# Optimization experiments

Measured on AMD Instinct MI355X. Metric: run time of the kernel, lower is better.

The kernel has to match this reference:

```python
import jax, jax.numpy as jnp
import numpy as np

N_NODES = 50000
N_EDGES = 800000
D_IN = 128
HIDDEN = [128, 128]
D_OUT = 64


def setup_inputs() -> dict:
    key = jax.random.key(0)
    ks = jax.random.split(key, 12)
    x = jax.random.normal(ks[0], (N_NODES, D_IN), dtype=jnp.float32)
    edge_index = jax.random.randint(ks[1], (2, N_EDGES), 0, N_NODES, dtype=jnp.int64)
    # SAGEConv params: lin_l acts on aggregated neighbors (has bias), lin_r on root
    def lin(k, fan_in, fan_out):
        s = 1.0 / np.sqrt(fan_in)
        return jax.random.uniform(k, (fan_in, fan_out), jnp.float32, -s, s)
    dims = [D_IN] + HIDDEN
    inp = {"x": x, "edge_index": edge_index}
    for i in range(len(HIDDEN)):
        inp[f"Wl{i}"] = lin(ks[2 + 3 * i], dims[i], dims[i + 1])
        inp[f"Wr{i}"] = lin(ks[3 + 3 * i], dims[i], dims[i + 1])
        inp[f"b{i}"] = jnp.zeros((dims[i + 1],), jnp.float32)
    inp["Wfc"] = lin(ks[10], HIDDEN[-1], D_OUT)
    inp["bfc"] = jnp.zeros((D_OUT,), jnp.float32)
    return inp


def _sage_conv(x, src, dst, n, Wl, Wr, b, deg_inv):
    # mean-aggregate source features into destination nodes
    agg = jax.ops.segment_sum(x[src], dst, num_segments=n) * deg_inv[:, None]
    return agg @ Wl + x @ Wr + b


def reference(x, edge_index, Wl0, Wr0, b0, Wl1, Wr1, b1, Wfc, bfc):
    src, dst = edge_index[0], edge_index[1]
    n = x.shape[0]
    deg = jax.ops.segment_sum(jnp.ones((src.shape[0],), x.dtype), dst, num_segments=n)
    deg_inv = 1.0 / jnp.maximum(deg, 1.0)
    h = jax.nn.relu(_sage_conv(x, src, dst, n, Wl0, Wr0, b0, deg_inv))
    # dropout p=0 / eval mode -> identity
    h = jax.nn.relu(_sage_conv(h, src, dst, n, Wl1, Wr1, b1, deg_inv))
    return h @ Wfc + bfc
```

## Files before the change

### kernel.cpp

```cpp
#include <hip/hip_runtime.h>
#include <hip/hip_bf16.h>

#define NN 50000
#define NE 800000
#define D 128
#define DOUT 64
#define PAD 64
#define BSH 8
#define NBUCK 196
#define CAP 4608
#define CHUNK 4096

typedef __attribute__((ext_vector_type(8))) short short8;
typedef __attribute__((ext_vector_type(4))) float float4v;


__device__ inline unsigned short f2bf(float f) {
    union { float f; unsigned int i; } c; c.f = f;
    unsigned int u = c.i;
    return (unsigned short)((u + 0x7fffu + ((u >> 16) & 1u)) >> 16);
}
__device__ inline float bflo(unsigned int u) {
    union { unsigned int i; float f; } c; c.i = u << 16; return c.f;
}
__device__ inline float bfhi(unsigned int u) {
    union { unsigned int i; float f; } c; c.i = u & 0xffff0000u; return c.f;
}


__global__ void cast_f32_bf16(const float* __restrict__ in, unsigned short* __restrict__ outb, int n8) {
    int i = blockIdx.x * 256 + threadIdx.x;
    if (i >= n8) return;
    const float4* p = (const float4*)in + (size_t)i * 2;
    float4 a = p[0], b = p[1];
    unsigned int w0 = f2bf(a.x) | ((unsigned int)f2bf(a.y) << 16);
    unsigned int w1 = f2bf(a.z) | ((unsigned int)f2bf(a.w) << 16);
    unsigned int w2 = f2bf(b.x) | ((unsigned int)f2bf(b.y) << 16);
    unsigned int w3 = f2bf(b.z) | ((unsigned int)f2bf(b.w) << 16);
    *(uint4*)(outb + (size_t)i * 8) = make_uint4(w0, w1, w2, w3);
}


struct PackArgs {
    const float* W[5];
    unsigned short* P[5];
};

__global__ void pack_all(PackArgs args) {
    int idx = blockIdx.x * 256 + threadIdx.x;
    if (idx >= 4 * 2048 + 1024) return;
    const float* W;
    unsigned short* P;
    int COLS, local;
    if (idx < 4 * 2048) {
        int wsel = idx >> 11;
        W = args.W[wsel]; P = args.P[wsel]; COLS = 128; local = idx & 2047;
    } else {
        W = args.W[4]; P = args.P[4]; COLS = 64; local = idx - 4 * 2048;
    }
    int CT = COLS >> 4;
    int lane = local & 63;
    int fi = local >> 6;
    int ct = fi % CT;
    int kstep = fi / CT;
    int krow = kstep * 32 + (lane >> 4) * 8;
    int col = ct * 16 + (lane & 15);
    unsigned short v[8];
#pragma unroll
    for (int j = 0; j < 8; ++j) v[j] = f2bf(W[(size_t)(krow + j) * COLS + col]);
    unsigned int w0 = v[0] | ((unsigned int)v[1] << 16);
    unsigned int w1 = v[2] | ((unsigned int)v[3] << 16);
    unsigned int w2 = v[4] | ((unsigned int)v[5] << 16);
    unsigned int w3 = v[6] | ((unsigned int)v[7] << 16);
    *(uint4*)(P + (size_t)local * 8) = make_uint4(w0, w1, w2, w3);
}


__global__ void bin_edges(const int* __restrict__ src, const int* __restrict__ dst,
                          int* __restrict__ gcur, unsigned int* __restrict__ binned, int e) {
    __shared__ int cnt[NBUCK];
    __shared__ int sh[256];
    __shared__ int baseg[NBUCK];
    __shared__ int lcur[NBUCK];
    __shared__ unsigned int buf[CHUNK];
    int tid = threadIdx.x;
    int base = blockIdx.x * CHUNK;
    for (int b = tid; b < NBUCK; b += 256) cnt[b] = 0;
    __syncthreads();
    unsigned int rec[16];
#pragma unroll
    for (int i = 0; i < 16; ++i) {
        int ei = base + i * 256 + tid;
        rec[i] = 0xffffffffu;
        if (ei < e) {
            unsigned int d = (unsigned int)dst[ei];
            unsigned int s = (unsigned int)src[ei];
            rec[i] = (d << 16) | s;
            atomicAdd(&cnt[d >> BSH], 1);
        }
    }
    __syncthreads();
    int v = (tid < NBUCK) ? cnt[tid] : 0;
    sh[tid] = v;
    __syncthreads();
    for (int off = 1; off < 256; off <<= 1) {
        int t = (tid >= off) ? sh[tid - off] : 0;
        __syncthreads();
        sh[tid] += t;
        __syncthreads();
    }
    if (tid < NBUCK) {
        baseg[tid] = atomicAdd(&gcur[tid], cnt[tid]);
        lcur[tid] = sh[tid] - cnt[tid];
    }
    __syncthreads();
    int total = sh[255];
#pragma unroll
    for (int i = 0; i < 16; ++i) {
        if (rec[i] != 0xffffffffu) {
            int b = rec[i] >> 24;
            int pos = atomicAdd(&lcur[b], 1);
            buf[pos] = rec[i];
        }
    }
    __syncthreads();
    for (int j = tid; j < total; j += 256) {
        unsigned int r = buf[j];
        int b = r >> 24;
        int gidx = baseg[b] + (j - (sh[b] - cnt[b]));
        if (gidx < CAP) binned[(size_t)b * CAP + gidx] = r;
    }
}


__global__ void scatter_bucket(const unsigned int* __restrict__ binned, const int* __restrict__ gcur,
                               unsigned short* __restrict__ eidx_pad, int* __restrict__ cursor) {
    __shared__ int cur[256];
    int b = blockIdx.x;
    int tid = threadIdx.x;
    cur[tid] = 0;
    __syncthreads();
    int count = gcur[b];
    if (count > CAP) count = CAP;
    const unsigned int* seg = binned + (size_t)b * CAP;
    for (int j = tid; j < count; j += 256) {
        unsigned int r = seg[j];
        int dl = (r >> 16) & 255;
        int slot = atomicAdd(&cur[dl], 1);
        if (slot < PAD)
            eidx_pad[((size_t)((b << BSH) + dl)) * PAD + slot] = (unsigned short)(r & 0xffffu);
    }
    __syncthreads();
    int node = (b << BSH) + tid;
    if (node < NN) cursor[node] = (cur[tid] < PAD) ? cur[tid] : PAD;
}


template <bool FUSEFC>
__global__ void fused_layer(const unsigned short* __restrict__ feat,
                            const int* __restrict__ cursor, const unsigned short* __restrict__ eidx_pad,
                            const unsigned short* __restrict__ Pl, const unsigned short* __restrict__ Pr,
                            const float* __restrict__ bias,
                            const unsigned short* __restrict__ Pfc, const float* __restrict__ bfc,
                            unsigned short* __restrict__ outb, float* __restrict__ outf, int n) {
    __shared__ __align__(16) unsigned short As[64][136];
    __shared__ __align__(16) unsigned short Xs[64][136];

    int tid = threadIdx.x;
    int row0 = blockIdx.x * 64;

    for (int v = tid; v < 1024; v += 256) {
        int r = v >> 4;
        int c8 = (v & 15) * 8;
        int gr = row0 + r;
        uint4 xv = make_uint4(0, 0, 0, 0);
        if (gr < n) xv = *(const uint4*)(feat + (size_t)gr * D + c8);
        *(uint4*)&Xs[r][c8] = xv;
    }

    {
        int g = tid >> 4;
        int l = tid & 15;
#pragma unroll
        for (int nn = 0; nn < 4; ++nn) {
            int r = g * 4 + nn;
            int node = row0 + r;
            float acc[8] = {0.f, 0.f, 0.f, 0.f, 0.f, 0.f, 0.f, 0.f};
            float di = 1.f;
            if (node < n) {
                int deg = cursor[node];
                di = 1.0f / (float)(deg > 1 ? deg : 1);
                const unsigned short* rowp = eidx_pad + (size_t)node * PAD;
                int p = 0;
                for (; p + 3 < deg; p += 4) {
                    int s0 = rowp[p], s1 = rowp[p + 1], s2 = rowp[p + 2], s3 = rowp[p + 3];
                    uint4 v0 = *(const uint4*)(feat + (size_t)s0 * D + l * 8);
                    uint4 v1 = *(const uint4*)(feat + (size_t)s1 * D + l * 8);
                    uint4 v2 = *(const uint4*)(feat + (size_t)s2 * D + l * 8);
                    uint4 v3 = *(const uint4*)(feat + (size_t)s3 * D + l * 8);
                    acc[0] += (bflo(v0.x) + bflo(v1.x)) + (bflo(v2.x) + bflo(v3.x));
                    acc[1] += (bfhi(v0.x) + bfhi(v1.x)) + (bfhi(v2.x) + bfhi(v3.x));
                    acc[2] += (bflo(v0.y) + bflo(v1.y)) + (bflo(v2.y) + bflo(v3.y));
                    acc[3] += (bfhi(v0.y) + bfhi(v1.y)) + (bfhi(v2.y) + bfhi(v3.y));
                    acc[4] += (bflo(v0.z) + bflo(v1.z)) + (bflo(v2.z) + bflo(v3.z));
                    acc[5] += (bfhi(v0.z) + bfhi(v1.z)) + (bfhi(v2.z) + bfhi(v3.z));
                    acc[6] += (bflo(v0.w) + bflo(v1.w)) + (bflo(v2.w) + bflo(v3.w));
                    acc[7] += (bfhi(v0.w) + bfhi(v1.w)) + (bfhi(v2.w) + bfhi(v3.w));
                }
                for (; p < deg; ++p) {
                    int s = rowp[p];
                    uint4 v0 = *(const uint4*)(feat + (size_t)s * D + l * 8);
                    acc[0] += bflo(v0.x); acc[1] += bfhi(v0.x);
                    acc[2] += bflo(v0.y); acc[3] += bfhi(v0.y);
                    acc[4] += bflo(v0.z); acc[5] += bfhi(v0.z);
                    acc[6] += bflo(v0.w); acc[7] += bfhi(v0.w);
                }
            }
            unsigned int w0 = f2bf(acc[0] * di) | ((unsigned int)f2bf(acc[1] * di) << 16);
            unsigned int w1 = f2bf(acc[2] * di) | ((unsigned int)f2bf(acc[3] * di) << 16);
            unsigned int w2 = f2bf(acc[4] * di) | ((unsigned int)f2bf(acc[5] * di) << 16);
            unsigned int w3 = f2bf(acc[6] * di) | ((unsigned int)f2bf(acc[7] * di) << 16);
            *(uint4*)&As[r][l * 8] = make_uint4(w0, w1, w2, w3);
        }
    }
    __syncthreads();

    int wave = tid >> 6;
    int lane = tid & 63;
    int m16 = lane & 15;
    int quad = lane >> 4;
    int rt0 = (wave & 1) * 32;
    int ctb = (wave >> 1) * 4;

    float4v acc[2][4];
#pragma unroll
    for (int t = 0; t < 2; ++t)
#pragma unroll
        for (int c = 0; c < 4; ++c) acc[t][c] = (float4v){0.f, 0.f, 0.f, 0.f};

#pragma unroll
    for (int ks = 0; ks < 4; ++ks) {
        short8 af[2];
#pragma unroll
        for (int t = 0; t < 2; ++t)
            af[t] = *(const short8*)&As[rt0 + t * 16 + m16][ks * 32 + quad * 8];
#pragma unroll
        for (int c = 0; c < 4; ++c) {
            short8 bf = *(const short8*)(Pl + ((size_t)((ks * 8 + ctb + c) * 64 + lane)) * 8);
#pragma unroll
            for (int t = 0; t < 2; ++t)
                acc[t][c] = __builtin_amdgcn_mfma_f32_16x16x32_bf16(af[t], bf, acc[t][c], 0, 0, 0);
        }
    }
#pragma unroll
    for (int ks = 0; ks < 4; ++ks) {
        short8 xf[2];
#pragma unroll
        for (int t = 0; t < 2; ++t)
            xf[t] = *(const short8*)&Xs[rt0 + t * 16 + m16][ks * 32 + quad * 8];
#pragma unroll
        for (int c = 0; c < 4; ++c) {
            short8 bf = *(const short8*)(Pr + ((size_t)((ks * 8 + ctb + c) * 64 + lane)) * 8);
#pragma unroll
            for (int t = 0; t < 2; ++t)
                acc[t][c] = __builtin_amdgcn_mfma_f32_16x16x32_bf16(xf[t], bf, acc[t][c], 0, 0, 0);
        }
    }

    if (!FUSEFC) {
#pragma unroll
        for (int t = 0; t < 2; ++t) {
#pragma unroll
            for (int c = 0; c < 4; ++c) {
                int col = (ctb + c) * 16 + m16;
                float bv = bias[col];
#pragma unroll
                for (int i = 0; i < 4; ++i) {
                    int row = row0 + rt0 + t * 16 + quad * 4 + i;
                    if (row < n)
                        outb[(size_t)row * D + col] = f2bf(fmaxf(acc[t][c][i] + bv, 0.f));
                }
            }
        }
    } else {
        __syncthreads();
#pragma unroll
        for (int t = 0; t < 2; ++t) {
#pragma unroll
            for (int c = 0; c < 4; ++c) {
                int col = (ctb + c) * 16 + m16;
                float bv = bias[col];
#pragma unroll
                for (int i = 0; i < 4; ++i) {
                    int row = rt0 + t * 16 + quad * 4 + i;
                    As[row][col] = f2bf(fmaxf(acc[t][c][i] + bv, 0.f));
                }
            }
        }
        __syncthreads();

        int ctbF = (wave >> 1) * 2;
        float4v acc2[2][2];
#pragma unroll
        for (int t = 0; t < 2; ++t)
#pragma unroll
            for (int c = 0; c < 2; ++c) acc2[t][c] = (float4v){0.f, 0.f, 0.f, 0.f};
#pragma unroll
        for (int ks = 0; ks < 4; ++ks) {
            short8 hf[2];
#pragma unroll
            for (int t = 0; t < 2; ++t)
                hf[t] = *(const short8*)&As[rt0 + t * 16 + m16][ks * 32 + quad * 8];
#pragma unroll
            for (int c = 0; c < 2; ++c) {
                short8 bf = *(const short8*)(Pfc + ((size_t)((ks * 4 + ctbF + c) * 64 + lane)) * 8);
#pragma unroll
                for (int t = 0; t < 2; ++t)
                    acc2[t][c] = __builtin_amdgcn_mfma_f32_16x16x32_bf16(hf[t], bf, acc2[t][c], 0, 0, 0);
            }
        }
#pragma unroll
        for (int t = 0; t < 2; ++t) {
#pragma unroll
            for (int c = 0; c < 2; ++c) {
                int col = (ctbF + c) * 16 + m16;
                float bv = bfc[col];
#pragma unroll
                for (int i = 0; i < 4; ++i) {
                    int row = row0 + rt0 + t * 16 + quad * 4 + i;
                    if (row < n)
                        outf[(size_t)row * DOUT + col] = acc2[t][c][i] + bv;
                }
            }
        }
    }
}


extern "C" void kernel_launch(void* const* d_in, const int* in_sizes, int n_in,
                              void* d_out, int out_size, void* d_ws, size_t ws_size,
                              hipStream_t stream) {
    const float* x   = (const float*)d_in[0];
    const int*   ei  = (const int*)d_in[1];
    const float* Wl0 = (const float*)d_in[2];
    const float* Wr0 = (const float*)d_in[3];
    const float* b0  = (const float*)d_in[4];
    const float* Wl1 = (const float*)d_in[5];
    const float* Wr1 = (const float*)d_in[6];
    const float* b1  = (const float*)d_in[7];
    const float* Wfc = (const float*)d_in[8];
    const float* bfc = (const float*)d_in[9];
    float* out = (float*)d_out;

    const int* src = ei;
    const int* dst = ei + NE;

    char* p = (char*)d_ws;
    auto carve = [&](size_t bytes) {
        char* q = p;
        p += (bytes + 255) & ~(size_t)255;
        return q;
    };
    int*            cursor   = (int*)carve(NN * sizeof(int));
    int*            gcur     = (int*)carve(NBUCK * sizeof(int));
    unsigned int*   binned   = (unsigned int*)carve((size_t)NBUCK * CAP * 4);
    unsigned short* eidx_pad = (unsigned short*)carve((size_t)NN * PAD * 2);
    unsigned short* xb   = (unsigned short*)carve((size_t)NN * D * 2);
    unsigned short* h0b  = (unsigned short*)carve((size_t)NN * D * 2);
    unsigned short* Wl0p = (unsigned short*)carve(D * D * 2);
    unsigned short* Wr0p = (unsigned short*)carve(D * D * 2);
    unsigned short* Wl1p = (unsigned short*)carve(D * D * 2);
    unsigned short* Wr1p = (unsigned short*)carve(D * D * 2);
    unsigned short* Wfcp = (unsigned short*)carve(D * DOUT * 2);

    hipMemsetAsync(gcur, 0, NBUCK * sizeof(int), stream);

    const int N8 = NN * D / 8;
    cast_f32_bf16<<<(N8 + 255) / 256, 256, 0, stream>>>(x, xb, N8);

    PackArgs pa;
    pa.W[0] = Wl0; pa.W[1] = Wr0; pa.W[2] = Wl1; pa.W[3] = Wr1; pa.W[4] = Wfc;
    pa.P[0] = Wl0p; pa.P[1] = Wr0p; pa.P[2] = Wl1p; pa.P[3] = Wr1p; pa.P[4] = Wfcp;
    pack_all<<<(4 * 2048 + 1024 + 255) / 256, 256, 0, stream>>>(pa);

    const int BINB = (NE + CHUNK - 1) / CHUNK;
    bin_edges<<<BINB, 256, 0, stream>>>(src, dst, gcur, binned, NE);
    scatter_bucket<<<NBUCK, 256, 0, stream>>>(binned, gcur, eidx_pad, cursor);

    const int GB = (NN + 63) / 64;

    fused_layer<false><<<GB, 256, 0, stream>>>(xb, cursor, eidx_pad, Wl0p, Wr0p, b0,
                                               nullptr, nullptr, h0b, nullptr, NN);
    fused_layer<true><<<GB, 256, 0, stream>>>(h0b, cursor, eidx_pad, Wl1p, Wr1p, b1,
                                              Wfcp, bfc, nullptr, out, NN);
}
```

Measured before the change: 199.1 us.

## Drop Xs LDS tile, widen neighbor gather, fold gcur reset into pack kernel

Several changes at once. The Xs shared-memory tile is removed and root features are read directly from global memory as MFMA operands, which halves LDS use so more blocks fit per CU; launch bounds of 4 blocks per CU are set to match. The gather loop now loads 8 neighbor indices with one vector load and issues 8 feature loads per iteration for more memory-level parallelism. The hipMemsetAsync of the bucket counters is replaced by an extra block in pack_all, removing one launch. The risks are higher register pressure from the wider unroll and uncoalesced global reads for the root operand.

New measurement: 199.0 us. About the same (-0.1%).

```diff
diff --git a/kernel.cpp b/kernel.cpp
--- a/kernel.cpp
+++ b/kernel.cpp
@@ -44,9 +44,14 @@
 struct PackArgs {
     const float* W[5];
     unsigned short* P[5];
+    int* gcur;
 };
 
 __global__ void pack_all(PackArgs args) {
+    if (blockIdx.x == 36) {
+        if (threadIdx.x < NBUCK) args.gcur[threadIdx.x] = 0;
+        return;
+    }
     int idx = blockIdx.x * 256 + threadIdx.x;
     if (idx >= 4 * 2048 + 1024) return;
     const float* W;
@@ -157,26 +162,17 @@
 
 
 template <bool FUSEFC>
-__global__ void fused_layer(const unsigned short* __restrict__ feat,
-                            const int* __restrict__ cursor, const unsigned short* __restrict__ eidx_pad,
-                            const unsigned short* __restrict__ Pl, const unsigned short* __restrict__ Pr,
-                            const float* __restrict__ bias,
-                            const unsigned short* __restrict__ Pfc, const float* __restrict__ bfc,
-                            unsigned short* __restrict__ outb, float* __restrict__ outf, int n) {
+__global__ __launch_bounds__(256, 4)
+void fused_layer(const unsigned short* __restrict__ feat,
+                 const int* __restrict__ cursor, const unsigned short* __restrict__ eidx_pad,
+                 const unsigned short* __restrict__ Pl, const unsigned short* __restrict__ Pr,
+                 const float* __restrict__ bias,
+                 const unsigned short* __restrict__ Pfc, const float* __restrict__ bfc,
+                 unsigned short* __restrict__ outb, float* __restrict__ outf, int n) {
     __shared__ __align__(16) unsigned short As[64][136];
-    __shared__ __align__(16) unsigned short Xs[64][136];
 
     int tid = threadIdx.x;
     int row0 = blockIdx.x * 64;
-
-    for (int v = tid; v < 1024; v += 256) {
-        int r = v >> 4;
-        int c8 = (v & 15) * 8;
-        int gr = row0 + r;
-        uint4 xv = make_uint4(0, 0, 0, 0);
-        if (gr < n) xv = *(const uint4*)(feat + (size_t)gr * D + c8);
-        *(uint4*)&Xs[r][c8] = xv;
-    }
 
     {
         int g = tid >> 4;
@@ -192,8 +188,41 @@
                 di = 1.0f / (float)(deg > 1 ? deg : 1);
                 const unsigned short* rowp = eidx_pad + (size_t)node * PAD;
                 int p = 0;
-                for (; p + 3 < deg; p += 4) {
-                    int s0 = rowp[p], s1 = rowp[p + 1], s2 = rowp[p + 2], s3 = rowp[p + 3];
+                for (; p + 7 < deg; p += 8) {
+                    uint4 iv = *(const uint4*)(rowp + p);
+                    int s0 = iv.x & 0xffff, s1 = iv.x >> 16;
+                    int s2 = iv.y & 0xffff, s3 = iv.y >> 16;
+                    int s4 = iv.z & 0xffff, s5 = iv.z >> 16;
+                    int s6 = iv.w & 0xffff, s7 = iv.w >> 16;
+                    uint4 v0 = *(const uint4*)(feat + (size_t)s0 * D + l * 8);
+                    uint4 v1 = *(const uint4*)(feat + (size_t)s1 * D + l * 8);
+                    uint4 v2 = *(const uint4*)(feat + (size_t)s2 * D + l * 8);
+                    uint4 v3 = *(const uint4*)(feat + (size_t)s3 * D + l * 8);
+                    uint4 v4 = *(const uint4*)(feat + (size_t)s4 * D + l * 8);
+                    uint4 v5 = *(const uint4*)(feat + (size_t)s5 * D + l * 8);
+                    uint4 v6 = *(const uint4*)(feat + (size_t)s6 * D + l * 8);
+                    uint4 v7 = *(const uint4*)(feat + (size_t)s7 * D + l * 8);
+                    acc[0] += ((bflo(v0.x) + bflo(v1.x)) + (bflo(v2.x) + bflo(v3.x)))
+                            + ((bflo(v4.x) + bflo(v5.x)) + (bflo(v6.x) + bflo(v7.x)));
+                    acc[1] += ((bfhi(v0.x) + bfhi(v1.x)) + (bfhi(v2.x) + bfhi(v3.x)))
+                            + ((bfhi(v4.x) + bfhi(v5.x)) + (bfhi(v6.x) + bfhi(v7.x)));
+                    acc[2] += ((bflo(v0.y) + bflo(v1.y)) + (bflo(v2.y) + bflo(v3.y)))
+                            + ((bflo(v4.y) + bflo(v5.y)) + (bflo(v6.y) + bflo(v7.y)));
+                    acc[3] += ((bfhi(v0.y) + bfhi(v1.y)) + (bfhi(v2.y) + bfhi(v3.y)))
+                            + ((bfhi(v4.y) + bfhi(v5.y)) + (bfhi(v6.y) + bfhi(v7.y)));
+                    acc[4] += ((bflo(v0.z) + bflo(v1.z)) + (bflo(v2.z) + bflo(v3.z)))
+                            + ((bflo(v4.z) + bflo(v5.z)) + (bflo(v6.z) + bflo(v7.z)));
+                    acc[5] += ((bfhi(v0.z) + bfhi(v1.z)) + (bfhi(v2.z) + bfhi(v3.z)))
+                            + ((bfhi(v4.z) + bfhi(v5.z)) + (bfhi(v6.z) + bfhi(v7.z)));
+                    acc[6] += ((bflo(v0.w) + bflo(v1.w)) + (bflo(v2.w) + bflo(v3.w)))
+                            + ((bflo(v4.w) + bflo(v5.w)) + (bflo(v6.w) + bflo(v7.w)));
+                    acc[7] += ((bfhi(v0.w) + bfhi(v1.w)) + (bfhi(v2.w) + bfhi(v3.w)))
+                            + ((bfhi(v4.w) + bfhi(v5.w)) + (bfhi(v6.w) + bfhi(v7.w)));
+                }
+                if (p + 3 < deg) {
+                    uint2 iv = *(const uint2*)(rowp + p);
+                    int s0 = iv.x & 0xffff, s1 = iv.x >> 16;
+                    int s2 = iv.y & 0xffff, s3 = iv.y >> 16;
                     uint4 v0 = *(const uint4*)(feat + (size_t)s0 * D + l * 8);
                     uint4 v1 = *(const uint4*)(feat + (size_t)s1 * D + l * 8);
                     uint4 v2 = *(const uint4*)(feat + (size_t)s2 * D + l * 8);
@@ -206,6 +235,7 @@
                     acc[5] += (bfhi(v0.z) + bfhi(v1.z)) + (bfhi(v2.z) + bfhi(v3.z));
                     acc[6] += (bflo(v0.w) + bflo(v1.w)) + (bflo(v2.w) + bflo(v3.w));
                     acc[7] += (bfhi(v0.w) + bfhi(v1.w)) + (bfhi(v2.w) + bfhi(v3.w));
+                    p += 4;
                 }
                 for (; p < deg; ++p) {
                     int s = rowp[p];
@@ -256,8 +286,11 @@
     for (int ks = 0; ks < 4; ++ks) {
         short8 xf[2];
 #pragma unroll
-        for (int t = 0; t < 2; ++t)
-            xf[t] = *(const short8*)&Xs[rt0 + t * 16 + m16][ks * 32 + quad * 8];
+        for (int t = 0; t < 2; ++t) {
+            int row = row0 + rt0 + t * 16 + m16;
+            short8 z = {0, 0, 0, 0, 0, 0, 0, 0};
+            xf[t] = (row < n) ? *(const short8*)(feat + (size_t)row * D + ks * 32 + quad * 8) : z;
+        }
 #pragma unroll
         for (int c = 0; c < 4; ++c) {
             short8 bf = *(const short8*)(Pr + ((size_t)((ks * 8 + ctb + c) * 64 + lane)) * 8);
@@ -373,15 +406,14 @@
     unsigned short* Wr1p = (unsigned short*)carve(D * D * 2);
     unsigned short* Wfcp = (unsigned short*)carve(D * DOUT * 2);
 
-    hipMemsetAsync(gcur, 0, NBUCK * sizeof(int), stream);
-
     const int N8 = NN * D / 8;
     cast_f32_bf16<<<(N8 + 255) / 256, 256, 0, stream>>>(x, xb, N8);
 
     PackArgs pa;
     pa.W[0] = Wl0; pa.W[1] = Wr0; pa.W[2] = Wl1; pa.W[3] = Wr1; pa.W[4] = Wfc;
     pa.P[0] = Wl0p; pa.P[1] = Wr0p; pa.P[2] = Wl1p; pa.P[3] = Wr1p; pa.P[4] = Wfcp;
-    pack_all<<<(4 * 2048 + 1024 + 255) / 256, 256, 0, stream>>>(pa);
+    pa.gcur = gcur;
+    pack_all<<<37, 256, 0, stream>>>(pa);
 
     const int BINB = (NE + CHUNK - 1) / CHUNK;
     bin_edges<<<BINB, 256, 0, stream>>>(src, dst, gcur, binned, NE);
```
